# Optimization experiments

Hardware: AMD Instinct MI355X
Metric: run time of the kernel (lower is better)

## Reference

```python
import jax, jax.numpy as jnp
import numpy as np

DIM = 128
N_GNN = 3
B, N1, N2 = 8, 128, 512
VDW_N = 6.0
DEV_VDW = 0.2
MAX_VDW, MIN_VDW = 0.0356, 0.0178
DM_MIN = 0.5


def setup_inputs() -> dict:
    key = jax.random.key(0)
    ks = jax.random.split(key, 24)
    f32 = jnp.float32
    h1 = jax.random.normal(ks[0], (B, N1, 54), f32)
    h2 = jax.random.normal(ks[1], (B, N2, 54), f32)
    a1 = (jax.random.uniform(ks[2], (B, N1, N1)) < 0.1).astype(f32)
    adj1 = jnp.clip(a1 + jnp.swapaxes(a1, 1, 2) + jnp.eye(N1, dtype=f32), 0.0, 1.0)
    a2 = (jax.random.uniform(ks[3], (B, N2, N2)) < 0.05).astype(f32)
    adj2 = jnp.clip(a2 + jnp.swapaxes(a2, 1, 2) + jnp.eye(N2, dtype=f32), 0.0, 1.0)
    A_int = (jax.random.uniform(ks[4], (B, 8, N1, N2)) < 0.05).astype(f32)
    pos1 = jax.random.uniform(ks[5], (B, N1, 3), f32) * 30.0
    pos2 = jax.random.uniform(ks[6], (B, N2, 3), f32) * 30.0
    rotor = jax.random.uniform(ks[7], (B,), f32) * 10.0
    vdw_radius1 = 1.0 + jax.random.uniform(ks[8], (B, N1), f32)
    vdw_radius2 = 1.0 + jax.random.uniform(ks[9], (B, N2), f32)
    delta_uff = jax.random.uniform(ks[10], (B,), f32)
    no_metal1 = jnp.ones((B, N1), f32)
    no_metal2 = jnp.ones((B, N2), f32)
    s = 0.1
    node_W = jax.random.normal(ks[11], (54, DIM), f32) * s
    gat_W = jax.random.normal(ks[12], (N_GNN, DIM, DIM), f32) * s
    gat_b = jnp.zeros((N_GNN, DIM), f32)
    gat_A = jax.random.normal(ks[13], (N_GNN, DIM, DIM), f32) * s
    gate_W = jax.random.normal(ks[14], (N_GNN, 2 * DIM), f32) * s
    gate_b = jnp.zeros((N_GNN,), f32)
    vdwA_W1 = jax.random.normal(ks[15], (2 * DIM, 128), f32) * s
    vdwA_b1 = jnp.zeros((128,), f32)
    vdwA_W2 = jax.random.normal(ks[16], (128,), f32) * s
    vdwA_b2 = jnp.zeros((1,), f32)
    vdwB_W1 = jax.random.normal(ks[17], (2 * DIM, 128), f32) * s
    vdwB_b1 = jnp.zeros((128,), f32)
    vdwB_W2 = jax.random.normal(ks[18], (128,), f32) * s
    vdwB_b2 = jnp.zeros((1,), f32)
    hbond_coeff = jnp.array([1.0], f32)
    hydrophobic_coeff = jnp.array([0.5], f32)
    vdw_coeff = jnp.array([1.0], f32)
    rotor_coeff = jnp.array([0.5], f32)
    return dict(h1=h1, adj1=adj1, h2=h2, adj2=adj2, A_int=A_int, pos1=pos1, pos2=pos2,
                rotor=rotor, vdw_radius1=vdw_radius1, vdw_radius2=vdw_radius2,
                delta_uff=delta_uff, no_metal1=no_metal1, no_metal2=no_metal2,
                node_W=node_W, gat_W=gat_W, gat_b=gat_b, gat_A=gat_A, gate_W=gate_W,
                gate_b=gate_b, vdwA_W1=vdwA_W1, vdwA_b1=vdwA_b1, vdwA_W2=vdwA_W2,
                vdwA_b2=vdwA_b2, vdwB_W1=vdwB_W1, vdwB_b1=vdwB_b1, vdwB_W2=vdwB_W2,
                vdwB_b2=vdwB_b2, hbond_coeff=hbond_coeff,
                hydrophobic_coeff=hydrophobic_coeff, vdw_coeff=vdw_coeff,
                rotor_coeff=rotor_coeff)


def _gat(x, adj, W, b, A, gW, gb):
    # PIGNet GAT_gate: attention softmax over axis=1, masked by adj, gated residual.
    h = x @ W + b                                   # [B,N,D]
    e = jnp.einsum('bil,bkl->bik', h @ A, h)        # [B,N,N]
    e = e + jnp.swapaxes(e, 1, 2)
    att = jnp.where(adj > 0, e, -9e15)
    att = jax.nn.softmax(att, axis=1) * adj
    h_prime = jax.nn.relu(jnp.einsum('bij,bjk->bik', att, h))
    coeff = jax.nn.sigmoid(jnp.concatenate([x, h_prime], -1) @ gW + gb)[..., None]
    return coeff * x + (1.0 - coeff) * h_prime


def _pair_mlp(g1, g2, W1, b1, w2, b2):
    # Equivalent to Linear(cat[h1_rep,h2_rep]) without materializing the 2D concat.
    z = (jnp.einsum('bik,kh->bih', g1, W1[:DIM])[:, :, None, :]
         + jnp.einsum('bjk,kh->bjh', g2, W1[DIM:])[:, None, :, :] + b1)  # [B,N1,N2,128]
    return jax.nn.relu(z) @ w2 + b2                 # [B,N1,N2]


def _forward(h1, adj1, h2, adj2, A_int, pos1, pos2, rotor, vdw_radius1, vdw_radius2,
             delta_uff, no_metal1, no_metal2, node_W, gat_W, gat_b, gat_A, gate_W,
             gate_b, vdwA_W1, vdwA_b1, vdwA_W2, vdwA_b2, vdwB_W1, vdwB_b1, vdwB_W2,
             vdwB_b2, hbond_coeff, hydrophobic_coeff, vdw_coeff, rotor_coeff):
    g1 = h1 @ node_W
    g2 = h2 @ node_W
    for i in range(N_GNN):
        g1 = _gat(g1, adj1, gat_W[i], gat_b[i], gat_A[i], gate_W[i], gate_b[i])
        g2 = _gat(g2, adj2, gat_W[i], gat_b[i], gat_A[i], gate_W[i], gate_b[i])
    diff = pos1[:, :, None, :] - pos2[:, None, :, :]
    dm = jnp.sqrt(jnp.sum(diff * diff, -1) + 1e-10)   # [B,N1,N2]
    dm = jnp.where(dm < DM_MIN, 1e10, dm)
    A_w = jax.nn.sigmoid(_pair_mlp(g1, g2, vdwA_W1, vdwA_b1, vdwA_W2, vdwA_b2))
    B_w = jnp.tanh(_pair_mlp(g1, g2, vdwB_W1, vdwB_b1, vdwB_W2, vdwB_b2)) * DEV_VDW
    dm0 = vdw_radius1[:, :, None] + vdw_radius2[:, None, :] + B_w
    # vdW 12-6 term
    dm0_safe = jnp.where(dm0 < 1e-4, 1.0, dm0)
    rN = (dm0_safe / dm) ** VDW_N
    evdw = jnp.minimum(rN * rN - 2.0 * rN, 100.0)
    mask12 = no_metal1[:, :, None] * no_metal2[:, None, :]
    Aamp = A_w * (MAX_VDW - MIN_VDW) + MIN_VDW
    E_vdw = jnp.sum(Aamp * evdw * mask12, axis=(1, 2))
    # hbond / hydrophobic terms use unfixed dm0
    dmd = dm - dm0
    hb = -(hbond_coeff * hbond_coeff)[0]
    hy = -(hydrophobic_coeff * hydrophobic_coeff)[0]
    E_hb1 = jnp.sum(jnp.clip(dmd * A_int[:, 1] / -0.7, 0.0, 1.0), axis=(1, 2)) * hb
    E_hb2 = jnp.sum(jnp.clip(dmd * A_int[:, -1] / -0.7, 0.0, 1.0), axis=(1, 2)) * hb
    E_hp = jnp.sum(jnp.clip((-dmd + 1.5) * A_int[:, -2], 0.0, 1.0), axis=(1, 2)) * hy
    E_t = delta_uff * (vdw_coeff * vdw_coeff)[0]
    ret = jnp.stack([E_vdw, E_hb1, E_hb2, E_hp, E_t], -1)   # [B,5]
    ret = ret / (1.0 + (rotor_coeff * rotor_coeff)[0] * rotor[:, None])
    return ret


def reference(h1, adj1, h2, adj2, A_int, pos1, pos2, rotor, vdw_radius1, vdw_radius2,
              delta_uff, no_metal1, no_metal2, node_W, gat_W, gat_b, gat_A, gate_W,
              gate_b, vdwA_W1, vdwA_b1, vdwA_W2, vdwA_b2, vdwB_W1, vdwB_b1, vdwB_W2,
              vdwB_b2, hbond_coeff, hydrophobic_coeff, vdw_coeff, rotor_coeff):
    return _forward(h1, adj1, h2, adj2, A_int, pos1, pos2, rotor, vdw_radius1,
                    vdw_radius2, delta_uff, no_metal1, no_metal2, node_W, gat_W,
                    gat_b, gat_A, gate_W, gate_b, vdwA_W1, vdwA_b1, vdwA_W2,
                    vdwA_b2, vdwB_W1, vdwB_b1, vdwB_W2, vdwB_b2, hbond_coeff,
                    hydrophobic_coeff, vdw_coeff, rotor_coeff)
```

## Files before the change

### kernel.cpp

```cpp
#include <hip/hip_runtime.h>
#include <math.h>

#define D 128
#define NB 8
#define NN1 128
#define NN2 512
#define ROWS1 (NB * NN1)
#define ROWS2 (NB * NN2)
#define ROWS (ROWS1 + ROWS2)
#define CAP1 96
#define CAP2 160
#define CSR_ELEMS ((size_t)ROWS1 * CAP1 + (size_t)ROWS2 * CAP2)

__device__ __forceinline__ void resolve_row(int row, int& base_row, size_t& cbase,
                                            int& N) {
    if (row < ROWS1) {
        base_row = row & ~127;
        cbase = (size_t)row * CAP1;
        N = NN1;
    } else {
        int r = row - ROWS1;
        base_row = ROWS1 + (r & ~511);
        cbase = (size_t)ROWS1 * CAP1 + (size_t)r * CAP2;
        N = NN2;
    }
}

__global__ __launch_bounds__(128) void k_csrembed(
    const float* __restrict__ h1, const float* __restrict__ h2,
    const float* __restrict__ adj1, const float* __restrict__ adj2,
    const float* __restrict__ W, float* __restrict__ g,
    unsigned short* __restrict__ csr, int* __restrict__ nnz) {
    int row = blockIdx.x;
    int t = threadIdx.x;
    const float* src = (row < ROWS1) ? h1 + (size_t)row * 54
                                     : h2 + (size_t)(row - ROWS1) * 54;
    __shared__ float xr[56];
    if (t < 54) xr[t] = src[t];
    __syncthreads();
    float a0 = 0.f, a1 = 0.f;
#pragma unroll
    for (int k = 0; k < 54; k += 2) {
        a0 += xr[k] * W[k * D + t];
        if (k + 1 < 54) a1 += xr[k + 1] * W[(k + 1) * D + t];
    }
    g[(size_t)row * D + t] = a0 + a1;

    if (t < 64) {
        int base_row, N;
        size_t cbase;
        resolve_row(row, base_row, cbase, N);
        int cap = (row < ROWS1) ? CAP1 : CAP2;
        const float* arow = (row < ROWS1)
                                ? adj1 + (size_t)row * NN1
                                : adj2 + (size_t)(row - ROWS1) * NN2;
        int cnt = 0;
        for (int c0 = 0; c0 < N; c0 += 64) {
            float v = arow[c0 + t];
            unsigned long long m = __ballot(v > 0.f);
            int rank = __popcll(m & ((1ull << t) - 1ull));
            if (v > 0.f && cnt + rank < cap)
                csr[cbase + cnt + rank] = (unsigned short)(c0 + t);
            cnt += __popcll(m);
        }
        if (t == 0) nnz[row] = cnt < cap ? cnt : cap;
    }
}

__global__ __launch_bounds__(256) void k_h(const float* __restrict__ g,
                                           const float* __restrict__ W,
                                           const float* __restrict__ bias,
                                           const float* __restrict__ A,
                                           float* __restrict__ h, float* __restrict__ hA) {
    int row0 = blockIdx.x * 16;
    int t = threadIdx.x;
    int d = t & 127, rh = t >> 7;
    __shared__ float xs[16][D];
    __shared__ float hs[16][D];
    {
        int r = t >> 4, c = (t & 15) * 8;
        *(float4*)&xs[r][c] = *(const float4*)&g[((size_t)row0 + r) * D + c];
        *(float4*)&xs[r][c + 4] = *(const float4*)&g[((size_t)row0 + r) * D + c + 4];
    }
    __syncthreads();
    float bv = bias[d];
    float acc[8];
#pragma unroll
    for (int u = 0; u < 8; ++u) acc[u] = bv;
    for (int k0 = 0; k0 < D; k0 += 4) {
        float w0 = W[(k0 + 0) * D + d];
        float w1 = W[(k0 + 1) * D + d];
        float w2 = W[(k0 + 2) * D + d];
        float w3 = W[(k0 + 3) * D + d];
#pragma unroll
        for (int u = 0; u < 8; ++u) {
            float4 xv = *(const float4*)&xs[rh * 8 + u][k0];
            acc[u] += xv.x * w0 + xv.y * w1 + xv.z * w2 + xv.w * w3;
        }
    }
#pragma unroll
    for (int u = 0; u < 8; ++u) {
        int r = rh * 8 + u;
        h[((size_t)row0 + r) * D + d] = acc[u];
        hs[r][d] = acc[u];
    }
    __syncthreads();
    float acc2[8];
#pragma unroll
    for (int u = 0; u < 8; ++u) acc2[u] = 0.f;
    for (int k0 = 0; k0 < D; k0 += 4) {
        float w0 = A[(k0 + 0) * D + d];
        float w1 = A[(k0 + 1) * D + d];
        float w2 = A[(k0 + 2) * D + d];
        float w3 = A[(k0 + 3) * D + d];
#pragma unroll
        for (int u = 0; u < 8; ++u) {
            float4 xv = *(const float4*)&hs[rh * 8 + u][k0];
            acc2[u] += xv.x * w0 + xv.y * w1 + xv.z * w2 + xv.w * w3;
        }
    }
#pragma unroll
    for (int u = 0; u < 8; ++u)
        hA[((size_t)row0 + rh * 8 + u) * D + d] = acc2[u];
}

__global__ __launch_bounds__(128) void k_Ssp(const float* __restrict__ h,
                                             const float* __restrict__ hA,
                                             const unsigned short* __restrict__ csr,
                                             const int* __restrict__ nnz,
                                             float* __restrict__ svals,
                                             float2* __restrict__ rowstat) {
    int row = blockIdx.x;
    int t = threadIdx.x;
    int base_row, N;
    size_t cbase;
    resolve_row(row, base_row, cbase, N);
    int n = nnz[row];
    int grp = t >> 4, u = t & 15;
    const float* hrow = h + (size_t)row * D + u * 8;
    const float* hArow = hA + (size_t)row * D + u * 8;
    float4 hi0 = *(const float4*)&hrow[0], hi1 = *(const float4*)&hrow[4];
    float4 ai0 = *(const float4*)&hArow[0], ai1 = *(const float4*)&hArow[4];
    __shared__ float sv[CAP2];
    for (int s0 = 0; s0 < n; s0 += 8) {
        int s = s0 + grp;
        float p = 0.f;
        if (s < n) {
            int jrow = base_row + csr[cbase + s];
            const float* hj = h + (size_t)jrow * D + u * 8;
            const float* aj = hA + (size_t)jrow * D + u * 8;
            float4 hj0 = *(const float4*)&hj[0], hj1 = *(const float4*)&hj[4];
            float4 aj0 = *(const float4*)&aj[0], aj1 = *(const float4*)&aj[4];
            p = hi0.x * aj0.x + hi0.y * aj0.y + hi0.z * aj0.z + hi0.w * aj0.w +
                hi1.x * aj1.x + hi1.y * aj1.y + hi1.z * aj1.z + hi1.w * aj1.w +
                ai0.x * hj0.x + ai0.y * hj0.y + ai0.z * hj0.z + ai0.w * hj0.w +
                ai1.x * hj1.x + ai1.y * hj1.y + ai1.z * hj1.z + ai1.w * hj1.w;
        }
#pragma unroll
        for (int o = 8; o > 0; o >>= 1) p += __shfl_xor(p, o);
        if (s < n && u == 0) sv[s] = p;
    }
    __syncthreads();
    if (t < 64) {
        float m = -3.4e38f;
        for (int s = t; s < n; s += 64) m = fmaxf(m, sv[s]);
#pragma unroll
        for (int o = 32; o > 0; o >>= 1) m = fmaxf(m, __shfl_xor(m, o));
        float sum = 0.f;
        for (int s = t; s < n; s += 64) sum += expf(sv[s] - m);
#pragma unroll
        for (int o = 32; o > 0; o >>= 1) sum += __shfl_xor(sum, o);
        if (t == 0) rowstat[row] = make_float2(m, 1.f / sum);
    }
    for (int s = t; s < n; s += 128) svals[cbase + s] = sv[s];
}

__global__ __launch_bounds__(128) void k_hpgate(const float* __restrict__ hbuf,
                                                float* __restrict__ g,
                                                const float* __restrict__ svals,
                                                const float2* __restrict__ rowstat,
                                                const unsigned short* __restrict__ csr,
                                                const int* __restrict__ nnz,
                                                const float* __restrict__ gW,
                                                const float* __restrict__ gb) {
    int row = blockIdx.x;
    int d = threadIdx.x;
    int base_row, N;
    size_t cbase;
    resolve_row(row, base_row, cbase, N);
    int n = nnz[row];
    __shared__ float avals[CAP2];
    __shared__ int aidx[CAP2];
    __shared__ float red[128];
    for (int s = d; s < n; s += 128) {
        int jrow = base_row + csr[cbase + s];
        float2 st = rowstat[jrow];
        avals[s] = expf(svals[cbase + s] - st.x) * st.y;
        aidx[s] = jrow;
    }
    __syncthreads();
    float a0 = 0.f, a1 = 0.f, a2 = 0.f, a3 = 0.f;
    int s = 0;
    for (; s + 4 <= n; s += 4) {
        a0 += avals[s + 0] * hbuf[(size_t)aidx[s + 0] * D + d];
        a1 += avals[s + 1] * hbuf[(size_t)aidx[s + 1] * D + d];
        a2 += avals[s + 2] * hbuf[(size_t)aidx[s + 2] * D + d];
        a3 += avals[s + 3] * hbuf[(size_t)aidx[s + 3] * D + d];
    }
    for (; s < n; ++s) a0 += avals[s] * hbuf[(size_t)aidx[s] * D + d];
    float hv = fmaxf(a0 + a1 + a2 + a3, 0.f);
    float xv = g[(size_t)row * D + d];
    red[d] = xv * gW[d] + hv * gW[D + d];
    __syncthreads();
    for (int o = 64; o > 0; o >>= 1) {
        if (d < o) red[d] += red[d + o];
        __syncthreads();
    }
    float c = 1.f / (1.f + expf(-(red[0] + gb[0])));
    g[(size_t)row * D + d] = c * xv + (1.f - c) * hv;
}

__global__ __launch_bounds__(256) void k_pairpre(const float* __restrict__ g,
                                                 const float* __restrict__ WA,
                                                 const float* __restrict__ WB,
                                                 const float* __restrict__ bA,
                                                 const float* __restrict__ bB,
                                                 float* __restrict__ aA,
                                                 float* __restrict__ aB) {
    int row0 = blockIdx.x * 16;
    int t = threadIdx.x;
    int d = t & 127, rh = t >> 7;
    int g2 = (row0 >= ROWS1);
    const float* WAp = g2 ? WA + D * D : WA;
    const float* WBp = g2 ? WB + D * D : WB;
    __shared__ float xs[16][D];
    {
        int r = t >> 4, c = (t & 15) * 8;
        *(float4*)&xs[r][c] = *(const float4*)&g[((size_t)row0 + r) * D + c];
        *(float4*)&xs[r][c + 4] = *(const float4*)&g[((size_t)row0 + r) * D + c + 4];
    }
    __syncthreads();
    float bvA = g2 ? 0.f : bA[d];
    float bvB = g2 ? 0.f : bB[d];
    float accA[8], accB[8];
#pragma unroll
    for (int u = 0; u < 8; ++u) { accA[u] = bvA; accB[u] = bvB; }
    for (int k0 = 0; k0 < D; k0 += 4) {
        float wa0 = WAp[(k0 + 0) * D + d], wa1 = WAp[(k0 + 1) * D + d];
        float wa2 = WAp[(k0 + 2) * D + d], wa3 = WAp[(k0 + 3) * D + d];
        float wb0 = WBp[(k0 + 0) * D + d], wb1 = WBp[(k0 + 1) * D + d];
        float wb2 = WBp[(k0 + 2) * D + d], wb3 = WBp[(k0 + 3) * D + d];
#pragma unroll
        for (int u = 0; u < 8; ++u) {
            float4 xv = *(const float4*)&xs[rh * 8 + u][k0];
            accA[u] += xv.x * wa0 + xv.y * wa1 + xv.z * wa2 + xv.w * wa3;
            accB[u] += xv.x * wb0 + xv.y * wb1 + xv.z * wb2 + xv.w * wb3;
        }
    }
#pragma unroll
    for (int u = 0; u < 8; ++u) {
        int r = rh * 8 + u;
        aA[((size_t)row0 + r) * D + d] = accA[u];
        aB[((size_t)row0 + r) * D + d] = accB[u];
    }
}

__global__ __launch_bounds__(256) void k_pairz(
    const float* __restrict__ aA, const float* __restrict__ aB,
    const float* __restrict__ w2A, const float* __restrict__ w2B,
    const float* __restrict__ b2A, const float* __restrict__ b2B,
    const float* __restrict__ pos1, const float* __restrict__ pos2,
    const float* __restrict__ vr1, const float* __restrict__ vr2,
    const float* __restrict__ nm1, const float* __restrict__ nm2,
    const float* __restrict__ A_int, float* __restrict__ partials) {
    int b = blockIdx.y;
    int itile = blockIdx.x >> 4, jtile = blockIdx.x & 15;
    int i0 = itile * 32, j0 = jtile * 32;
    int t = threadIdx.x;
    int tx = t & 15, ty = t >> 4;
    __shared__ float A1a[32][20], A1b[32][20], A2a[32][20], A2b[32][20];
    __shared__ float w2As[128], w2Bs[128];
    __shared__ float zAs[32][33], zBs[32][33];
    if (t < 128) { w2As[t] = w2A[t]; w2Bs[t] = w2B[t]; }
    float zA[2][2] = {{0.f, 0.f}, {0.f, 0.f}};
    float zB[2][2] = {{0.f, 0.f}, {0.f, 0.f}};
    int half = t >> 7, idx = t & 127;
    int sr = idx >> 2, sc = (idx & 3) * 4;
    size_t grow = half ? (size_t)(ROWS1 + b * NN2 + j0 + sr)
                       : (size_t)(b * NN1 + i0 + sr);
    for (int hc = 0; hc < D; hc += 16) {
        __syncthreads();
        float4 va = *(const float4*)&aA[grow * D + hc + sc];
        float4 vb = *(const float4*)&aB[grow * D + hc + sc];
        if (half) { *(float4*)&A2a[sr][sc] = va; *(float4*)&A2b[sr][sc] = vb; }
        else      { *(float4*)&A1a[sr][sc] = va; *(float4*)&A1b[sr][sc] = vb; }
        __syncthreads();
#pragma unroll
        for (int hh = 0; hh < 16; hh += 4) {
            float4 wA = *(const float4*)&w2As[hc + hh];
            float4 wB = *(const float4*)&w2Bs[hc + hh];
            float4 xA0 = *(const float4*)&A1a[ty][hh];
            float4 xA1 = *(const float4*)&A1a[ty + 16][hh];
            float4 xB0 = *(const float4*)&A1b[ty][hh];
            float4 xB1 = *(const float4*)&A1b[ty + 16][hh];
            float4 yA0 = *(const float4*)&A2a[tx][hh];
            float4 yA1 = *(const float4*)&A2a[tx + 16][hh];
            float4 yB0 = *(const float4*)&A2b[tx][hh];
            float4 yB1 = *(const float4*)&A2b[tx + 16][hh];
#define RD4(xx, yy, ww) (fmaxf(xx.x + yy.x, 0.f) * ww.x + fmaxf(xx.y + yy.y, 0.f) * ww.y + \
                         fmaxf(xx.z + yy.z, 0.f) * ww.z + fmaxf(xx.w + yy.w, 0.f) * ww.w)
            zA[0][0] += RD4(xA0, yA0, wA); zA[0][1] += RD4(xA0, yA1, wA);
            zA[1][0] += RD4(xA1, yA0, wA); zA[1][1] += RD4(xA1, yA1, wA);
            zB[0][0] += RD4(xB0, yB0, wB); zB[0][1] += RD4(xB0, yB1, wB);
            zB[1][0] += RD4(xB1, yB0, wB); zB[1][1] += RD4(xB1, yB1, wB);
#undef RD4
        }
    }
#pragma unroll
    for (int u = 0; u < 2; ++u)
#pragma unroll
        for (int v = 0; v < 2; ++v) {
            zAs[ty + 16 * u][tx + 16 * v] = zA[u][v];
            zBs[ty + 16 * u][tx + 16 * v] = zB[u][v];
        }
    __syncthreads();
    int j2 = t & 31, ig = t >> 5;
    int jg = j0 + j2;
    size_t j_off = (size_t)b * NN2 + jg;
    float p2x = pos2[j_off * 3 + 0], p2y = pos2[j_off * 3 + 1], p2z = pos2[j_off * 3 + 2];
    float r2 = vr2[j_off], m2 = nm2[j_off];
    float zb2A = b2A[0], zb2B = b2B[0];
    float eV[4], e1[4], e2[4], eH[4];
#pragma unroll
    for (int ii = 0; ii < 4; ++ii) {
        int il = ig * 4 + ii;
        int iglob = i0 + il;
        size_t i_off = (size_t)b * NN1 + iglob;
        float zAv = zAs[il][j2] + zb2A;
        float zBv = zBs[il][j2] + zb2B;
        float dx = pos1[i_off * 3 + 0] - p2x;
        float dy = pos1[i_off * 3 + 1] - p2y;
        float dz = pos1[i_off * 3 + 2] - p2z;
        float dm = sqrtf(dx * dx + dy * dy + dz * dz + 1e-10f);
        if (dm < 0.5f) dm = 1e10f;
        float A_w = 1.f / (1.f + expf(-zAv));
        float B_w = tanhf(zBv) * 0.2f;
        float dm0 = vr1[i_off] + r2 + B_w;
        float dm0s = (dm0 < 1e-4f) ? 1.f : dm0;
        float rr = dm0s / dm;
        float rr2 = rr * rr;
        float rN = rr2 * rr2 * rr2;
        float evdw = fminf(rN * rN - 2.f * rN, 100.f);
        float mask = nm1[i_off] * m2;
        float Aamp = A_w * (0.0356f - 0.0178f) + 0.0178f;
        eV[ii] = Aamp * evdw * mask;
        float dmd = dm - dm0;
        size_t abase = (((size_t)b * 8) * NN1 + iglob) * NN2 + jg;
        float Ai1 = A_int[abase + (size_t)1 * NN1 * NN2];
        float Ai6 = A_int[abase + (size_t)6 * NN1 * NN2];
        float Ai7 = A_int[abase + (size_t)7 * NN1 * NN2];
        e1[ii] = fminf(fmaxf(dmd * Ai1 * (-1.f / 0.7f), 0.f), 1.f);
        e2[ii] = fminf(fmaxf(dmd * Ai7 * (-1.f / 0.7f), 0.f), 1.f);
        eH[ii] = fminf(fmaxf((1.5f - dmd) * Ai6, 0.f), 1.f);
    }
#pragma unroll
    for (int o = 16; o > 0; o >>= 1) {
#pragma unroll
        for (int ii = 0; ii < 4; ++ii) {
            eV[ii] += __shfl_xor(eV[ii], o);
            e1[ii] += __shfl_xor(e1[ii], o);
            e2[ii] += __shfl_xor(e2[ii], o);
            eH[ii] += __shfl_xor(eH[ii], o);
        }
    }
    if (j2 == 0) {
#pragma unroll
        for (int ii = 0; ii < 4; ++ii) {
            int iglob = i0 + ig * 4 + ii;
            float* pp = partials + (((size_t)b * NN1 + iglob) * 16 + jtile) * 4;
            pp[0] = eV[ii]; pp[1] = e1[ii]; pp[2] = e2[ii]; pp[3] = eH[ii];
        }
    }
}

__global__ void k_final(const float* __restrict__ partials, const float* __restrict__ rotor,
                        const float* __restrict__ duff, const float* __restrict__ hbond,
                        const float* __restrict__ hydro, const float* __restrict__ vdwc,
                        const float* __restrict__ rotc, float* __restrict__ out) {
    int b = blockIdx.x;
    int t = threadIdx.x;
    __shared__ float r[4][128];
    float v0 = 0.f, v1 = 0.f, v2 = 0.f, v3 = 0.f;
    const float* p = partials + ((size_t)b * NN1 + t) * 16 * 4;
#pragma unroll
    for (int jt = 0; jt < 16; ++jt) {
        v0 += p[jt * 4 + 0]; v1 += p[jt * 4 + 1];
        v2 += p[jt * 4 + 2]; v3 += p[jt * 4 + 3];
    }
    r[0][t] = v0; r[1][t] = v1; r[2][t] = v2; r[3][t] = v3;
    __syncthreads();
    for (int s = 64; s > 0; s >>= 1) {
        if (t < s) {
            r[0][t] += r[0][t + s];
            r[1][t] += r[1][t + s];
            r[2][t] += r[2][t + s];
            r[3][t] += r[3][t + s];
        }
        __syncthreads();
    }
    if (t == 0) {
        float hb = -hbond[0] * hbond[0];
        float hy = -hydro[0] * hydro[0];
        float Et = duff[b] * vdwc[0] * vdwc[0];
        float sc = 1.f / (1.f + rotc[0] * rotc[0] * rotor[b]);
        out[b * 5 + 0] = r[0][0] * sc;
        out[b * 5 + 1] = r[1][0] * hb * sc;
        out[b * 5 + 2] = r[2][0] * hb * sc;
        out[b * 5 + 3] = r[3][0] * hy * sc;
        out[b * 5 + 4] = Et * sc;
    }
}

extern "C" void kernel_launch(void* const* d_in, const int* in_sizes, int n_in,
                              void* d_out, int out_size, void* d_ws, size_t ws_size,
                              hipStream_t stream) {
    const float* h1    = (const float*)d_in[0];
    const float* adj1  = (const float*)d_in[1];
    const float* h2    = (const float*)d_in[2];
    const float* adj2  = (const float*)d_in[3];
    const float* A_int = (const float*)d_in[4];
    const float* pos1  = (const float*)d_in[5];
    const float* pos2  = (const float*)d_in[6];
    const float* rotor = (const float*)d_in[7];
    const float* vr1   = (const float*)d_in[8];
    const float* vr2   = (const float*)d_in[9];
    const float* duff  = (const float*)d_in[10];
    const float* nm1   = (const float*)d_in[11];
    const float* nm2   = (const float*)d_in[12];
    const float* nodeW = (const float*)d_in[13];
    const float* gatW  = (const float*)d_in[14];
    const float* gatb  = (const float*)d_in[15];
    const float* gatA  = (const float*)d_in[16];
    const float* gateW = (const float*)d_in[17];
    const float* gateb = (const float*)d_in[18];
    const float* vA_W1 = (const float*)d_in[19];
    const float* vA_b1 = (const float*)d_in[20];
    const float* vA_W2 = (const float*)d_in[21];
    const float* vA_b2 = (const float*)d_in[22];
    const float* vB_W1 = (const float*)d_in[23];
    const float* vB_b1 = (const float*)d_in[24];
    const float* vB_W2 = (const float*)d_in[25];
    const float* vB_b2 = (const float*)d_in[26];
    const float* hbond = (const float*)d_in[27];
    const float* hydro = (const float*)d_in[28];
    const float* vdwc  = (const float*)d_in[29];
    const float* rotc  = (const float*)d_in[30];

    float* p = (float*)d_ws;
    float* g     = p; p += (size_t)ROWS * D;
    float* hbuf  = p; p += (size_t)ROWS * D;
    float* hAbuf = p; p += (size_t)ROWS * D;
    float* svals = p; p += CSR_ELEMS;
    float2* rowstat = (float2*)p; p += 2 * (size_t)ROWS;
    float* partials = p; p += (size_t)NB * NN1 * 16 * 4;
    unsigned short* csr = (unsigned short*)p;
    int* nnz = (int*)(csr + CSR_ELEMS);
    float* aA = hbuf;
    float* aB = hAbuf;

    k_csrembed<<<ROWS, 128, 0, stream>>>(h1, h2, adj1, adj2, nodeW, g, csr, nnz);

    for (int l = 0; l < 3; ++l) {
        const float* W  = gatW  + (size_t)l * D * D;
        const float* bb = gatb  + (size_t)l * D;
        const float* A  = gatA  + (size_t)l * D * D;
        const float* gW = gateW + (size_t)l * 2 * D;
        const float* gb = gateb + l;
        k_h<<<ROWS / 16, 256, 0, stream>>>(g, W, bb, A, hbuf, hAbuf);
        k_Ssp<<<ROWS, 128, 0, stream>>>(hbuf, hAbuf, csr, nnz, svals, rowstat);
        k_hpgate<<<ROWS, 128, 0, stream>>>(hbuf, g, svals, rowstat, csr, nnz, gW, gb);
    }

    k_pairpre<<<ROWS / 16, 256, 0, stream>>>(g, vA_W1, vB_W1, vA_b1, vB_b1, aA, aB);
    k_pairz<<<dim3(64, NB), 256, 0, stream>>>(aA, aB, vA_W2, vB_W2, vA_b2, vB_b2,
                                              pos1, pos2, vr1, vr2, nm1, nm2, A_int,
                                              partials);
    k_final<<<NB, 128, 0, stream>>>(partials, rotor, duff, hbond, hydro, vdwc, rotc,
                                    (float*)d_out);
}
```

Before: 312.6 us.

## Fuse final reduction into pair kernel via atomics and widen gather ILP

```diff
diff --git a/kernel.cpp b/kernel.cpp
--- a/kernel.cpp
+++ b/kernel.cpp
@@ -30,9 +30,11 @@
     const float* __restrict__ h1, const float* __restrict__ h2,
     const float* __restrict__ adj1, const float* __restrict__ adj2,
     const float* __restrict__ W, float* __restrict__ g,
-    unsigned short* __restrict__ csr, int* __restrict__ nnz) {
+    unsigned short* __restrict__ csr, int* __restrict__ nnz,
+    float* __restrict__ out) {
     int row = blockIdx.x;
     int t = threadIdx.x;
+    if (row == 0 && t < NB * 5) out[t] = 0.f;
     const float* src = (row < ROWS1) ? h1 + (size_t)row * 54
                                      : h2 + (size_t)(row - ROWS1) * 54;
     __shared__ float xr[56];
@@ -142,23 +144,41 @@
     float4 hi0 = *(const float4*)&hrow[0], hi1 = *(const float4*)&hrow[4];
     float4 ai0 = *(const float4*)&hArow[0], ai1 = *(const float4*)&hArow[4];
     __shared__ float sv[CAP2];
-    for (int s0 = 0; s0 < n; s0 += 8) {
-        int s = s0 + grp;
-        float p = 0.f;
-        if (s < n) {
-            int jrow = base_row + csr[cbase + s];
+    for (int s0 = 0; s0 < n; s0 += 16) {
+        int sa = s0 + grp;
+        int sb = sa + 8;
+        float pa = 0.f, pb = 0.f;
+        if (sa < n) {
+            int jrow = base_row + csr[cbase + sa];
             const float* hj = h + (size_t)jrow * D + u * 8;
             const float* aj = hA + (size_t)jrow * D + u * 8;
             float4 hj0 = *(const float4*)&hj[0], hj1 = *(const float4*)&hj[4];
             float4 aj0 = *(const float4*)&aj[0], aj1 = *(const float4*)&aj[4];
-            p = hi0.x * aj0.x + hi0.y * aj0.y + hi0.z * aj0.z + hi0.w * aj0.w +
-                hi1.x * aj1.x + hi1.y * aj1.y + hi1.z * aj1.z + hi1.w * aj1.w +
-                ai0.x * hj0.x + ai0.y * hj0.y + ai0.z * hj0.z + ai0.w * hj0.w +
-                ai1.x * hj1.x + ai1.y * hj1.y + ai1.z * hj1.z + ai1.w * hj1.w;
-        }
-#pragma unroll
-        for (int o = 8; o > 0; o >>= 1) p += __shfl_xor(p, o);
-        if (s < n && u == 0) sv[s] = p;
+            pa = hi0.x * aj0.x + hi0.y * aj0.y + hi0.z * aj0.z + hi0.w * aj0.w +
+                 hi1.x * aj1.x + hi1.y * aj1.y + hi1.z * aj1.z + hi1.w * aj1.w +
+                 ai0.x * hj0.x + ai0.y * hj0.y + ai0.z * hj0.z + ai0.w * hj0.w +
+                 ai1.x * hj1.x + ai1.y * hj1.y + ai1.z * hj1.z + ai1.w * hj1.w;
+        }
+        if (sb < n) {
+            int jrow = base_row + csr[cbase + sb];
+            const float* hj = h + (size_t)jrow * D + u * 8;
+            const float* aj = hA + (size_t)jrow * D + u * 8;
+            float4 hj0 = *(const float4*)&hj[0], hj1 = *(const float4*)&hj[4];
+            float4 aj0 = *(const float4*)&aj[0], aj1 = *(const float4*)&aj[4];
+            pb = hi0.x * aj0.x + hi0.y * aj0.y + hi0.z * aj0.z + hi0.w * aj0.w +
+                 hi1.x * aj1.x + hi1.y * aj1.y + hi1.z * aj1.z + hi1.w * aj1.w +
+                 ai0.x * hj0.x + ai0.y * hj0.y + ai0.z * hj0.z + ai0.w * hj0.w +
+                 ai1.x * hj1.x + ai1.y * hj1.y + ai1.z * hj1.z + ai1.w * hj1.w;
+        }
+#pragma unroll
+        for (int o = 8; o > 0; o >>= 1) {
+            pa += __shfl_xor(pa, o);
+            pb += __shfl_xor(pb, o);
+        }
+        if (u == 0) {
+            if (sa < n) sv[sa] = pa;
+            if (sb < n) sv[sb] = pb;
+        }
     }
     __syncthreads();
     if (t < 64) {
@@ -199,16 +219,18 @@
         aidx[s] = jrow;
     }
     __syncthreads();
-    float a0 = 0.f, a1 = 0.f, a2 = 0.f, a3 = 0.f;
+    float a[8];
+#pragma unroll
+    for (int u = 0; u < 8; ++u) a[u] = 0.f;
     int s = 0;
-    for (; s + 4 <= n; s += 4) {
-        a0 += avals[s + 0] * hbuf[(size_t)aidx[s + 0] * D + d];
-        a1 += avals[s + 1] * hbuf[(size_t)aidx[s + 1] * D + d];
-        a2 += avals[s + 2] * hbuf[(size_t)aidx[s + 2] * D + d];
-        a3 += avals[s + 3] * hbuf[(size_t)aidx[s + 3] * D + d];
-    }
-    for (; s < n; ++s) a0 += avals[s] * hbuf[(size_t)aidx[s] * D + d];
-    float hv = fmaxf(a0 + a1 + a2 + a3, 0.f);
+    for (; s + 8 <= n; s += 8) {
+#pragma unroll
+        for (int u = 0; u < 8; ++u)
+            a[u] += avals[s + u] * hbuf[(size_t)aidx[s + u] * D + d];
+    }
+    for (; s < n; ++s) a[0] += avals[s] * hbuf[(size_t)aidx[s] * D + d];
+    float hv = fmaxf(((a[0] + a[1]) + (a[2] + a[3])) + ((a[4] + a[5]) + (a[6] + a[7])),
+                     0.f);
     float xv = g[(size_t)row * D + d];
     red[d] = xv * gW[d] + hv * gW[D + d];
     __syncthreads();
@@ -272,7 +294,10 @@
     const float* __restrict__ pos1, const float* __restrict__ pos2,
     const float* __restrict__ vr1, const float* __restrict__ vr2,
     const float* __restrict__ nm1, const float* __restrict__ nm2,
-    const float* __restrict__ A_int, float* __restrict__ partials) {
+    const float* __restrict__ A_int, const float* __restrict__ rotor,
+    const float* __restrict__ duff, const float* __restrict__ hbond,
+    const float* __restrict__ hydro, const float* __restrict__ vdwc,
+    const float* __restrict__ rotc, float* __restrict__ out) {
     int b = blockIdx.y;
     int itile = blockIdx.x >> 4, jtile = blockIdx.x & 15;
     int i0 = itile * 32, j0 = jtile * 32;
@@ -281,6 +306,7 @@
     __shared__ float A1a[32][20], A1b[32][20], A2a[32][20], A2b[32][20];
     __shared__ float w2As[128], w2Bs[128];
     __shared__ float zAs[32][33], zBs[32][33];
+    __shared__ float redc[8][4];
     if (t < 128) { w2As[t] = w2A[t]; w2Bs[t] = w2B[t]; }
     float zA[2][2] = {{0.f, 0.f}, {0.f, 0.f}};
     float zB[2][2] = {{0.f, 0.f}, {0.f, 0.f}};
@@ -363,61 +389,35 @@
         e2[ii] = fminf(fmaxf(dmd * Ai7 * (-1.f / 0.7f), 0.f), 1.f);
         eH[ii] = fminf(fmaxf((1.5f - dmd) * Ai6, 0.f), 1.f);
     }
+    float sV = (eV[0] + eV[1]) + (eV[2] + eV[3]);
+    float s1 = (e1[0] + e1[1]) + (e1[2] + e1[3]);
+    float s2 = (e2[0] + e2[1]) + (e2[2] + e2[3]);
+    float sH = (eH[0] + eH[1]) + (eH[2] + eH[3]);
 #pragma unroll
     for (int o = 16; o > 0; o >>= 1) {
-#pragma unroll
-        for (int ii = 0; ii < 4; ++ii) {
-            eV[ii] += __shfl_xor(eV[ii], o);
-            e1[ii] += __shfl_xor(e1[ii], o);
-            e2[ii] += __shfl_xor(e2[ii], o);
-            eH[ii] += __shfl_xor(eH[ii], o);
-        }
+        sV += __shfl_xor(sV, o);
+        s1 += __shfl_xor(s1, o);
+        s2 += __shfl_xor(s2, o);
+        sH += __shfl_xor(sH, o);
     }
     if (j2 == 0) {
-#pragma unroll
-        for (int ii = 0; ii < 4; ++ii) {
-            int iglob = i0 + ig * 4 + ii;
-            float* pp = partials + (((size_t)b * NN1 + iglob) * 16 + jtile) * 4;
-            pp[0] = eV[ii]; pp[1] = e1[ii]; pp[2] = e2[ii]; pp[3] = eH[ii];
-        }
-    }
-}
-
-__global__ void k_final(const float* __restrict__ partials, const float* __restrict__ rotor,
-                        const float* __restrict__ duff, const float* __restrict__ hbond,
-                        const float* __restrict__ hydro, const float* __restrict__ vdwc,
-                        const float* __restrict__ rotc, float* __restrict__ out) {
-    int b = blockIdx.x;
-    int t = threadIdx.x;
-    __shared__ float r[4][128];
-    float v0 = 0.f, v1 = 0.f, v2 = 0.f, v3 = 0.f;
-    const float* p = partials + ((size_t)b * NN1 + t) * 16 * 4;
-#pragma unroll
-    for (int jt = 0; jt < 16; ++jt) {
-        v0 += p[jt * 4 + 0]; v1 += p[jt * 4 + 1];
-        v2 += p[jt * 4 + 2]; v3 += p[jt * 4 + 3];
-    }
-    r[0][t] = v0; r[1][t] = v1; r[2][t] = v2; r[3][t] = v3;
-    __syncthreads();
-    for (int s = 64; s > 0; s >>= 1) {
-        if (t < s) {
-            r[0][t] += r[0][t + s];
-            r[1][t] += r[1][t + s];
-            r[2][t] += r[2][t + s];
-            r[3][t] += r[3][t + s];
-        }
-        __syncthreads();
-    }
-    if (t == 0) {
-        float hb = -hbond[0] * hbond[0];
-        float hy = -hydro[0] * hydro[0];
-        float Et = duff[b] * vdwc[0] * vdwc[0];
-        float sc = 1.f / (1.f + rotc[0] * rotc[0] * rotor[b]);
-        out[b * 5 + 0] = r[0][0] * sc;
-        out[b * 5 + 1] = r[1][0] * hb * sc;
-        out[b * 5 + 2] = r[2][0] * hb * sc;
-        out[b * 5 + 3] = r[3][0] * hy * sc;
-        out[b * 5 + 4] = Et * sc;
+        redc[ig][0] = sV; redc[ig][1] = s1; redc[ig][2] = s2; redc[ig][3] = sH;
+    }
+    __syncthreads();
+    if (t < 4) {
+        float v = 0.f;
+#pragma unroll
+        for (int gg = 0; gg < 8; ++gg) v += redc[gg][t];
+        float scl = 1.f / (1.f + rotc[0] * rotc[0] * rotor[b]);
+        float coef;
+        if (t == 0) coef = scl;
+        else if (t == 3) coef = -hydro[0] * hydro[0] * scl;
+        else coef = -hbond[0] * hbond[0] * scl;
+        atomicAdd(&out[b * 5 + t], v * coef);
+    }
+    if (t == 4 && itile == 0 && jtile == 0) {
+        float scl = 1.f / (1.f + rotc[0] * rotc[0] * rotor[b]);
+        atomicAdd(&out[b * 5 + 4], duff[b] * vdwc[0] * vdwc[0] * scl);
     }
 }
 
@@ -462,13 +462,13 @@
     float* hAbuf = p; p += (size_t)ROWS * D;
     float* svals = p; p += CSR_ELEMS;
     float2* rowstat = (float2*)p; p += 2 * (size_t)ROWS;
-    float* partials = p; p += (size_t)NB * NN1 * 16 * 4;
     unsigned short* csr = (unsigned short*)p;
     int* nnz = (int*)(csr + CSR_ELEMS);
     float* aA = hbuf;
     float* aB = hAbuf;
 
-    k_csrembed<<<ROWS, 128, 0, stream>>>(h1, h2, adj1, adj2, nodeW, g, csr, nnz);
+    k_csrembed<<<ROWS, 128, 0, stream>>>(h1, h2, adj1, adj2, nodeW, g, csr, nnz,
+                                         (float*)d_out);
 
     for (int l = 0; l < 3; ++l) {
         const float* W  = gatW  + (size_t)l * D * D;
@@ -484,7 +484,6 @@
     k_pairpre<<<ROWS / 16, 256, 0, stream>>>(g, vA_W1, vB_W1, vA_b1, vB_b1, aA, aB);
     k_pairz<<<dim3(64, NB), 256, 0, stream>>>(aA, aB, vA_W2, vB_W2, vA_b2, vB_b2,
                                               pos1, pos2, vr1, vr2, nm1, nm2, A_int,
-                                              partials);
-    k_final<<<NB, 128, 0, stream>>>(partials, rotor, duff, hbond, hydro, vdwc, rotc,
-                                    (float*)d_out);
-}
+                                              rotor, duff, hbond, hydro, vdwc, rotc,
+                                              (float*)d_out);
+}
```

New measurement: 313.3 us. Within noise of the previous version (+0.2%).
